# Optimization experiments

Measured on AMD Instinct MI355X. Metric: run time of the kernel, lower is better.

The kernel has to match this reference:

```python
import jax, jax.numpy as jnp
import numpy as np

EPS = 1e-12  # matches torch F.normalize default eps
K = 10       # knn size hardcoded in forward


def _l2_normalize(x, axis):
    n = jnp.linalg.norm(x, axis=axis, keepdims=True)
    return x / jnp.maximum(n, EPS)


def setup_inputs() -> dict:
    key = jax.random.key(0)
    k1, k2, k3, k4, k5 = jax.random.split(key, 5)
    BS, D, C = 4096, 768, 128
    NCLUST, CSIZE, NTRAIN, NCLS = 500, 100, 100000, 10
    train_embedding = jax.random.normal(k1, (BS, D), dtype=jnp.float32)
    # init_concept: uniform in [-0.5, 0.5]
    concept = jax.random.uniform(k2, (D, C), dtype=jnp.float32, minval=-0.5, maxval=0.5)
    clusters = jax.random.normal(k3, (NCLUST, CSIZE, D), dtype=jnp.float32)
    train_embeddings = jax.random.normal(k4, (NTRAIN, D), dtype=jnp.float32)
    w_hx = jax.random.normal(k5, (NCLS, D), dtype=jnp.float32) * 0.02
    b_hx = jnp.zeros((NCLS,), dtype=jnp.float32)
    return {"train_embedding": train_embedding, "concept": concept,
            "clusters": clusters, "train_embeddings": train_embeddings,
            "w_hx": w_hx, "b_hx": b_hx}


def reference(train_embedding, concept, clusters, train_embeddings, w_hx, b_hx):
    C = concept.shape[1]
    E = train_embeddings.T                       # (D, N) == self.train_embeddings

    concept_normalized = _l2_normalize(concept, axis=0)
    gram = concept.T @ concept                   # (C, C)
    proj_matrix = concept @ jnp.linalg.inv(gram) @ concept.T   # (D, D)
    proj = proj_matrix @ train_embedding.T       # (D, BS)

    cluster_mean = jnp.mean(clusters, axis=1)    # (NCLUST, D)
    score_matrix = jnp.abs(cluster_mean @ concept_normalized)  # (NCLUST, C)
    score_norm = _l2_normalize(score_matrix, axis=0)
    L_sparse_1_old = jnp.sum(score_norm)
    # sum_{i!=j} dot(score_norm[:,i], score_norm[:,j]) = sum(G) - trace(G)
    G = score_norm.T @ score_norm                # (C, C)
    L_sparse_2_old = jnp.sum(G) - jnp.trace(G)

    y_pred = proj.T @ w_hx.T + b_hx              # (BS, NCLS)

    # batched knn over all concepts: ||e - c||^2 = ||e||^2 - 2 c.e + ||c||^2
    e_sq = jnp.sum(E * E, axis=0)                # (N,)
    c_sq = jnp.sum(concept * concept, axis=0)    # (C,)
    d2 = e_sq[None, :] - 2.0 * (concept.T @ E) + c_sq[:, None]  # (C, N)
    _, knn_idx = jax.lax.top_k(-d2, K)           # (C, K) smallest distances
    knn_act = E[:, knn_idx]                      # (D, C, K)
    # per-concept sum(c * c_knn)/K, then mean over concepts
    L_sparse_1_new = jnp.mean(jnp.sum(concept[:, :, None] * knn_act, axis=(0, 2)) / K)

    all_concept_dot = concept.T @ concept        # (C, C)
    mask = 1.0 - jnp.eye(C, dtype=all_concept_dot.dtype)
    L_sparse_2_new = jnp.mean(all_concept_dot * mask)

    return (y_pred, L_sparse_1_old, L_sparse_2_old, L_sparse_1_new, L_sparse_2_new)
```

## Files before the change

kernel.cpp:

```cpp
#include <hip/hip_runtime.h>
#include <stdint.h>

#define M_TRAIN 100000
#define D_DIM   768
#define C_DIM   128
#define NCLUST  500
#define CSIZE   100
#define NCLS    10
#define KSEL    10
#define NCHUNK  4
#define CHUNKN  25000
#define CAND_PER 16
#define NCT     (NCHUNK * CAND_PER)
#define FLT_INF 3.402823466e38f

typedef __attribute__((ext_vector_type(8))) short bhalf8;
typedef __attribute__((ext_vector_type(4))) float f32x4;
typedef __attribute__((ext_vector_type(8))) unsigned short ushort8;
typedef __attribute__((ext_vector_type(4))) unsigned short ushort4v;

#define WS_KEYT   0LL
#define WS_BIMG   25600000LL
#define WS_CONT   25796608LL
#define WS_GRAM   26189824LL
#define WS_PSCORE 26255360LL
#define WS_CT     26767360LL
#define WS_CAND   26798080LL
#define WS_PSUM   26830848LL
#define WS_TSOL   26831360LL

#define GSTR 132

static __device__ __forceinline__ unsigned short f2bf(float f) {
    union { float f; unsigned int u; } x; x.f = f;
    unsigned int u = x.u;
    return (unsigned short)((u + 0x7fffu + ((u >> 16) & 1u)) >> 16);
}

__global__ void __launch_bounds__(256) kA(const float* __restrict__ cpt,
        const float* __restrict__ clus, float* __restrict__ conceptT,
        unsigned short* __restrict__ bimg, float* __restrict__ gram,
        float* __restrict__ pscore) {
    int b = blockIdx.x, t = threadIdx.x;
    if (b < 1000) {
        __shared__ float mean_s[D_DIM];
        int cl = b >> 1, h = b & 1;
        if (t < 192) {
            const float* base = clus + (long)cl * CSIZE * D_DIM + (long)h * 50 * D_DIM + t * 4;
            float ax = 0.f, ay = 0.f, az = 0.f, aw = 0.f;
            for (int s = 0; s < 50; s += 2) {
                float4 v0 = *(const float4*)(base + (long)s * D_DIM);
                float4 v1 = *(const float4*)(base + (long)(s + 1) * D_DIM);
                ax += v0.x + v1.x; ay += v0.y + v1.y;
                az += v0.z + v1.z; aw += v0.w + v1.w;
            }
            const float k = 1.0f / CSIZE;
            mean_s[t * 4 + 0] = ax * k; mean_s[t * 4 + 1] = ay * k;
            mean_s[t * 4 + 2] = az * k; mean_s[t * 4 + 3] = aw * k;
        }
        __syncthreads();
        if (t < 128) {
            float s = 0.f;
            #pragma unroll 4
            for (int d = 0; d < D_DIM; ++d) s += mean_s[d] * cpt[d * 128 + t];
            pscore[h * (NCLUST * 128) + cl * 128 + t] = s;
        }
    } else if (b < 1384) {
        int tid = (b - 1000) * 256 + t;
        int d = tid >> 7, c = tid & 127;
        float v = cpt[tid];
        conceptT[c * D_DIM + d] = v;
        int kc = d >> 6, kin = d & 63;
        int ofs = kc * 16384 + (((c << 7) + (kin << 1)) ^ ((c & 7) << 4));
        *(unsigned short*)((char*)bimg + ofs) = f2bf(v);
    } else {
        int c1 = (b - 1384) * 2 + (t >> 7);
        int c2 = t & 127;
        float s = 0.f;
        #pragma unroll 4
        for (int d = 0; d < D_DIM; ++d)
            s += cpt[d * 128 + c1] * cpt[d * 128 + c2];
        gram[c1 * 128 + c2] = s;
    }
}

__device__ __forceinline__ float blk_red256(float v, float* buf, int t) {
    #pragma unroll
    for (int m = 32; m > 0; m >>= 1) v += __shfl_xor(v, m);
    if ((t & 63) == 0) buf[t >> 6] = v;
    __syncthreads();
    return buf[0] + buf[1] + buf[2] + buf[3];
}

__device__ __forceinline__ void cg_role(char* smem, const float* __restrict__ gram,
        const float* __restrict__ cpt, const float* __restrict__ whx,
        float* __restrict__ tsol, float* __restrict__ out_l2new, int j) {
    float* G    = (float*)smem;
    float* p_s  = (float*)(smem + 67584);
    float* rbuf = (float*)(smem + 68096);
    int t = threadIdx.x;
    int r = t & 127;
    bool lo = (t < 128);
    if (lo) {
        #pragma unroll 8
        for (int c = 0; c < 128; c += 4)
            *(float4*)&G[r * GSTR + c] = *(const float4*)&gram[r * 128 + c];
    }
    const float* wj = whx + j * D_DIM;
    float rhs = 0.f;
    if (lo) {
        for (int d = 0; d < D_DIM; d += 4)
            rhs += cpt[(d + 0) * 128 + r] * wj[d + 0]
                 + cpt[(d + 1) * 128 + r] * wj[d + 1]
                 + cpt[(d + 2) * 128 + r] * wj[d + 2]
                 + cpt[(d + 3) * 128 + r] * wj[d + 3];
    }
    float x = 0.f, res = rhs, p = rhs;
    if (lo) p_s[r] = p;
    float rr = blk_red256(lo ? res * res : 0.f, rbuf, t);
    __syncthreads();
    if (j == 0) {
        float s = 0.f;
        if (lo) {
            #pragma unroll 8
            for (int c = 0; c < 128; ++c) s += G[r * GSTR + c];
            s -= G[r * GSTR + r];
        }
        float tot = blk_red256(s, rbuf + 8, t);
        if (t == 0) out_l2new[0] = tot / 16384.0f;
    }
    for (int it = 0; it < 20; ++it) {
        float q = 0.f;
        if (lo) {
            #pragma unroll 8
            for (int c = 0; c < 128; c += 4) {
                float4 g  = *(const float4*)&G[r * GSTR + c];
                float4 pp = *(const float4*)&p_s[c];
                q += g.x * pp.x + g.y * pp.y + g.z * pp.z + g.w * pp.w;
            }
        }
        float pq = blk_red256(lo ? p * q : 0.f, rbuf + 4, t);
        float alpha = rr / pq;
        x += alpha * p;
        res -= alpha * q;
        float rrn = blk_red256(lo ? res * res : 0.f, rbuf, t);
        float beta = rrn / rr;
        rr = rrn;
        p = res + beta * p;
        if (lo) p_s[r] = p;
        __syncthreads();
    }
    if (lo) tsol[r * NCLS + j] = x;
}

__device__ __forceinline__ void old_role(char* smem, const float* __restrict__ pscore,
        const float* __restrict__ gram, float* __restrict__ out01) {
    float* ss2     = (float*)smem;
    float* sm2     = (float*)(smem + 1024);
    float* rcn_s   = (float*)(smem + 2048);
    float* wcomb   = (float*)(smem + 2560);
    float* redA    = (float*)(smem + 3072);
    float* redB    = (float*)(smem + 3584);
    float* wred4   = (float*)(smem + 4096);
    float* trace_s = (float*)(smem + 4112);
    const float* p0 = pscore;
    const float* p1 = pscore + NCLUST * 128;
    int t = threadIdx.x;
    int c = t & 127, w2 = t >> 7;
    if (t < 128) rcn_s[t] = 1.0f / fmaxf(sqrtf(gram[t * 129]), 1e-12f);
    __syncthreads();
    float rc = rcn_s[c];
    float ss = 0.f, sm = 0.f;
    for (int bb = 0; bb < 25; ++bb) {
        float a[10];
        #pragma unroll
        for (int k = 0; k < 10; ++k) {
            int cl = w2 + 2 * (10 * bb + k);
            a[k] = p0[cl * 128 + c] + p1[cl * 128 + c];
        }
        #pragma unroll
        for (int k = 0; k < 10; ++k) { float v = fabsf(a[k]) * rc; ss += v * v; sm += v; }
    }
    ss2[w2 * 128 + c] = ss; sm2[w2 * 128 + c] = sm;
    __syncthreads();
    if (t < 128) {
        float S = ss2[t] + ss2[128 + t];
        float M = sm2[t] + sm2[128 + t];
        float nn = fmaxf(sqrtf(S), 1e-12f);
        float iv = 1.0f / nn;
        wcomb[t] = rcn_s[t] * iv;
        redA[t] = M * iv;
        redB[t] = S * iv * iv;
    }
    __syncthreads();
    if (t < 64) {
        float a = redA[t] + redA[t + 64];
        float b2 = redB[t] + redB[t + 64];
        #pragma unroll
        for (int m = 32; m > 0; m >>= 1) { a += __shfl_xor(a, m); b2 += __shfl_xor(b2, m); }
        if (t == 0) { out01[0] = a; trace_s[0] = b2; }
    }
    __syncthreads();
    int w = t >> 6, lane = t & 63;
    float wc0 = wcomb[lane], wc1 = wcomb[lane + 64];
    float rsq = 0.f;
    for (int bb = 0; bb < 25; ++bb) {
        float a0[5], a1[5];
        #pragma unroll
        for (int k = 0; k < 5; ++k) {
            int cl = w + 4 * (5 * bb + k);
            a0[k] = p0[cl * 128 + lane] + p1[cl * 128 + lane];
            a1[k] = p0[cl * 128 + 64 + lane] + p1[cl * 128 + 64 + lane];
        }
        #pragma unroll
        for (int k = 0; k < 5; ++k) {
            float v = fabsf(a0[k]) * wc0 + fabsf(a1[k]) * wc1;
            #pragma unroll
            for (int m = 32; m > 0; m >>= 1) v += __shfl_xor(v, m);
            if (lane == 0) rsq += v * v;
        }
    }
    if (lane == 0) wred4[w] = rsq;
    __syncthreads();
    if (t == 0) out01[1] = wred4[0] + wred4[1] + wred4[2] + wred4[3] - trace_s[0];
}

__device__ __forceinline__ void P_role(char* smem, const float* __restrict__ E,
        const unsigned short* __restrict__ bimg, unsigned short* __restrict__ keyT,
        int blk) {
    char* lds = smem;
    float* esq_s = (float*)(smem + 65536);
    unsigned short* cst = (unsigned short*)lds;

    int t = threadIdx.x;
    int rowbase = blk * 128;
    int lane = t & 63, w = t >> 6;
    int wr = w >> 1, wc = w & 1;
    f32x4 acc[4][4];
    #pragma unroll
    for (int m = 0; m < 4; ++m)
        #pragma unroll
        for (int n = 0; n < 4; ++n) acc[m][n] = (f32x4){0.f, 0.f, 0.f, 0.f};
    float esq_p[4] = {0.f, 0.f, 0.f, 0.f};
    int g = t >> 3, k8 = t & 7;

    float4 a0[4], a1[4];
    bhalf8 breg[4];

    auto stage_issue = [&](int ks) {
        #pragma unroll
        for (int p = 0; p < 4; ++p) {
            int grow = rowbase + 32 * p + g;
            if (grow < M_TRAIN) {
                const float* src = E + (long)grow * D_DIM + ks * 64 + k8 * 8;
                a0[p] = *(const float4*)(src);
                a1[p] = *(const float4*)(src + 4);
            } else {
                a0[p] = make_float4(0.f, 0.f, 0.f, 0.f);
                a1[p] = make_float4(0.f, 0.f, 0.f, 0.f);
            }
        }
        const char* bs = (const char*)bimg + ks * 16384;
        #pragma unroll
        for (int i = 0; i < 4; ++i)
            breg[i] = *(const bhalf8*)(bs + (i * 256 + t) * 16);
    };
    auto stage_write = [&](int buf) {
        char* Ab = lds + buf * 16384;
        char* Bb = lds + 32768 + buf * 16384;
        #pragma unroll
        for (int p = 0; p < 4; ++p) {
            int row = 32 * p + g;
            float4 v0 = a0[p], v1 = a1[p];
            esq_p[p] += v0.x*v0.x + v0.y*v0.y + v0.z*v0.z + v0.w*v0.w
                      + v1.x*v1.x + v1.y*v1.y + v1.z*v1.z + v1.w*v1.w;
            bhalf8 h;
            h[0] = (short)f2bf(v0.x); h[1] = (short)f2bf(v0.y);
            h[2] = (short)f2bf(v0.z); h[3] = (short)f2bf(v0.w);
            h[4] = (short)f2bf(v1.x); h[5] = (short)f2bf(v1.y);
            h[6] = (short)f2bf(v1.z); h[7] = (short)f2bf(v1.w);
            int byte = (row * 128 + k8 * 16) ^ ((row & 7) << 4);
            *(bhalf8*)(Ab + byte) = h;
        }
        #pragma unroll
        for (int i = 0; i < 4; ++i)
            *(bhalf8*)(Bb + (i * 256 + t) * 16) = breg[i];
    };

    stage_issue(0);
    stage_write(0);
    __syncthreads();
    int cur = 0;
    for (int ks = 0; ks < 12; ++ks) {
        if (ks < 11) stage_issue(ks + 1);
        const char* Ab = lds + cur * 16384;
        const char* Bb = lds + 32768 + cur * 16384;
        bhalf8 af[4][2], bf[4][2];
        int kb = (lane >> 4) * 16;
        #pragma unroll
        for (int m = 0; m < 4; ++m) {
            int row = wr * 64 + m * 16 + (lane & 15);
            int b0 = row * 128, sw = (row & 7) << 4;
            af[m][0] = *(const bhalf8*)(Ab + ((b0 + kb) ^ sw));
            af[m][1] = *(const bhalf8*)(Ab + ((b0 + kb + 64) ^ sw));
        }
        #pragma unroll
        for (int n = 0; n < 4; ++n) {
            int c = wc * 64 + n * 16 + (lane & 15);
            int b0 = c * 128, sw = (c & 7) << 4;
            bf[n][0] = *(const bhalf8*)(Bb + ((b0 + kb) ^ sw));
            bf[n][1] = *(const bhalf8*)(Bb + ((b0 + kb + 64) ^ sw));
        }
        #pragma unroll
        for (int m = 0; m < 4; ++m)
            #pragma unroll
            for (int n = 0; n < 4; ++n) {
                acc[m][n] = __builtin_amdgcn_mfma_f32_16x16x32_bf16(af[m][0], bf[n][0], acc[m][n], 0, 0, 0);
                acc[m][n] = __builtin_amdgcn_mfma_f32_16x16x32_bf16(af[m][1], bf[n][1], acc[m][n], 0, 0, 0);
            }
        if (ks < 11) stage_write(cur ^ 1);
        __syncthreads();
        cur ^= 1;
    }
    #pragma unroll
    for (int p = 0; p < 4; ++p) {
        float v = esq_p[p];
        v += __shfl_xor(v, 1); v += __shfl_xor(v, 2); v += __shfl_xor(v, 4);
        if (k8 == 0) esq_s[32 * p + g] = v;
    }
    __syncthreads();
    #pragma unroll
    for (int m = 0; m < 4; ++m) {
        int r0 = wr * 64 + m * 16 + (lane >> 4) * 4;
        float e0 = esq_s[r0], e1 = esq_s[r0 + 1], e2 = esq_s[r0 + 2], e3 = esq_s[r0 + 3];
        #pragma unroll
        for (int n = 0; n < 4; ++n) {
            int c = wc * 64 + n * 16 + (lane & 15);
            ushort4v kv;
            kv[0] = f2bf(e0 - 2.f * acc[m][n][0]);
            kv[1] = f2bf(e1 - 2.f * acc[m][n][1]);
            kv[2] = f2bf(e2 - 2.f * acc[m][n][2]);
            kv[3] = f2bf(e3 - 2.f * acc[m][n][3]);
            *(ushort4v*)(cst + c * 136 + r0) = kv;
        }
    }
    __syncthreads();
    #pragma unroll
    for (int it = 0; it < 8; ++it) {
        int c = w * 32 + it * 4 + (lane >> 4);
        int r = (lane & 15) * 8;
        if (rowbase + r < M_TRAIN) {
            ushort8 v = *(const ushort8*)(cst + c * 136 + r);
            *(ushort8*)(keyT + (long)c * M_TRAIN + rowbase + r) = v;
        }
    }
}

__global__ void __launch_bounds__(256, 2) kB(const float* __restrict__ E,
        const unsigned short* __restrict__ bimg, unsigned short* __restrict__ keyT,
        const float* __restrict__ gram, const float* __restrict__ cpt,
        const float* __restrict__ whx, float* __restrict__ tsol,
        float* __restrict__ out_scal, const float* __restrict__ pscore) {
    __shared__ __align__(16) char smem[68160];
    int b = blockIdx.x;
    if (b < 10)       cg_role(smem, gram, cpt, whx, tsol, out_scal + 3, b);
    else if (b == 10) old_role(smem, pscore, gram, out_scal);
    else              P_role(smem, E, bimg, keyT, b - 11);
}

__global__ void __launch_bounds__(256) kC(const unsigned short* __restrict__ keyT,
        int* __restrict__ cand, const float* __restrict__ cpt,
        const float* __restrict__ tsol, float* __restrict__ ct) {
    int b = blockIdx.x, t = threadIdx.x;
    if (b < 512) {
        __shared__ int sk[2048];
        __shared__ int si[2048];
        __shared__ int wk[4]; __shared__ int wi[4], wsl[4];
        int c = b >> 2, h = b & 3;
        const unsigned short* col = keyT + (long)c * M_TRAIN + h * CHUNKN;
        int base = h * CHUNKN;
        int tk[8], ti[8];
        #pragma unroll
        for (int i = 0; i < 8; ++i) { tk[i] = 0x7fffffff; ti[i] = 0x7fffffff; }
        for (int i = t; i < CHUNKN / 8; i += 256) {
            ushort8 v = *(const ushort8*)(col + i * 8);
            int idx = base + i * 8;
            #pragma unroll
            for (int q = 0; q < 8; ++q) {
                int cv = (int)v[q]; int ci = idx + q;
                if (cv < tk[7] || (cv == tk[7] && ci < ti[7])) {
                    #pragma unroll
                    for (int jj = 0; jj < 8; ++jj) {
                        bool sw = (cv < tk[jj]) || (cv == tk[jj] && ci < ti[jj]);
                        int ok = tk[jj]; int oi = ti[jj];
                        if (sw) { tk[jj] = cv; ti[jj] = ci; cv = ok; ci = oi; }
                    }
                }
            }
        }
        #pragma unroll
        for (int i = 0; i < 8; ++i) { sk[t * 8 + i] = tk[i]; si[t * 8 + i] = ti[i]; }
        __syncthreads();
        int lane = t & 63, w = t >> 6;
        for (int sel = 0; sel < CAND_PER; ++sel) {
            int bk = 0x7fffffff, bi = 0x7fffffff, bs = -1;
            #pragma unroll
            for (int i = 0; i < 8; ++i) {
                int s = t * 8 + i;
                int v = sk[s];
                if (v < bk || (v == bk && si[s] < bi)) { bk = v; bi = si[s]; bs = s; }
            }
            #pragma unroll
            for (int m = 32; m > 0; m >>= 1) {
                int ok = __shfl_xor(bk, m); int oi = __shfl_xor(bi, m); int os = __shfl_xor(bs, m);
                if (ok < bk || (ok == bk && oi < bi)) { bk = ok; bi = oi; bs = os; }
            }
            if (lane == 0) { wk[w] = bk; wi[w] = bi; wsl[w] = bs; }
            __syncthreads();
            if (t == 0) {
                int fk = wk[0], fi = wi[0], fs = wsl[0];
                for (int i = 1; i < 4; ++i)
                    if (wk[i] < fk || (wk[i] == fk && wi[i] < fi)) { fk = wk[i]; fi = wi[i]; fs = wsl[i]; }
                cand[(c * NCHUNK + h) * CAND_PER + sel] = fi;
                sk[fs] = 0x7fffffff; si[fs] = 0x7fffffff;
            }
            __syncthreads();
        }
    } else {
        int idx = (b - 512) * 256 + t;
        int d = idx / NCLS, j = idx - d * NCLS;
        const float* crow = cpt + d * 128;
        float s = 0.f;
        #pragma unroll 4
        for (int c = 0; c < 128; ++c) s += crow[c] * tsol[c * NCLS + j];
        ct[idx] = s;
    }
}

__global__ void __launch_bounds__(256) kD(const float* __restrict__ te,
        const float* __restrict__ ct, const float* __restrict__ bhx,
        float* __restrict__ out, const float* __restrict__ E,
        const float* __restrict__ conceptT, const int* __restrict__ cand,
        float* __restrict__ psum) {
    int b = blockIdx.x, t = threadIdx.x;
    if (b < 512) {
        __shared__ float ctT[NCLS][D_DIM];
        for (int o = t; o < D_DIM * NCLS; o += 256) {
            int j = o / D_DIM, d = o % D_DIM;
            ctT[j][d] = ct[d * NCLS + j];
        }
        __syncthreads();
        int r = t >> 5, l = t & 31;
        long row = (long)b * 8 + r;
        const float* er = te + row * D_DIM;
        float acc[NCLS];
        #pragma unroll
        for (int j = 0; j < NCLS; ++j) acc[j] = 0.f;
        for (int d0 = l * 4; d0 < D_DIM; d0 += 128) {
            float4 e = *(const float4*)(er + d0);
            #pragma unroll
            for (int j = 0; j < NCLS; ++j) {
                float4 cc = *(const float4*)(&ctT[j][d0]);
                acc[j] += e.x*cc.x + e.y*cc.y + e.z*cc.z + e.w*cc.w;
            }
        }
        #pragma unroll
        for (int j = 0; j < NCLS; ++j) {
            #pragma unroll
            for (int m = 16; m > 0; m >>= 1) acc[j] += __shfl_xor(acc[j], m);
        }
        if (l == 0) {
            #pragma unroll
            for (int j = 0; j < NCLS; ++j) out[row * NCLS + j] = acc[j] + bhx[j];
        }
    } else {
        __shared__ float skey[NCT], sdot[NCT];
        __shared__ int sidx[NCT];
        int c = b - 512;
        int g = t >> 2, l4 = t & 3;
        int idx = cand[c * NCT + g];
        const float* er = E + (long)idx * D_DIM;
        const float* cr = conceptT + c * D_DIM;
        float dot = 0.f, ss = 0.f;
        for (int d0 = l4 * 4; d0 < D_DIM; d0 += 16) {
            float4 e = *(const float4*)(er + d0);
            float4 cc = *(const float4*)(cr + d0);
            dot += e.x*cc.x + e.y*cc.y + e.z*cc.z + e.w*cc.w;
            ss  += e.x*e.x + e.y*e.y + e.z*e.z + e.w*e.w;
        }
        dot += __shfl_xor(dot, 1); dot += __shfl_xor(dot, 2);
        ss  += __shfl_xor(ss, 1);  ss  += __shfl_xor(ss, 2);
        if (l4 == 0) { skey[g] = ss - 2.f * dot; sdot[g] = dot; sidx[g] = idx; }
        __syncthreads();
        if (t == 0) {
            float sum = 0.f;
            unsigned long long used = 0ull;
            for (int s = 0; s < KSEL; ++s) {
                float bk = FLT_INF; int bi = 0x7fffffff, bs = 0;
                for (int i = 0; i < NCT; ++i) {
                    if ((used >> i) & 1ull) continue;
                    if (skey[i] < bk || (skey[i] == bk && sidx[i] < bi)) { bk = skey[i]; bi = sidx[i]; bs = i; }
                }
                used |= (1ull << bs);
                sum += sdot[bs];
            }
            psum[c] = sum;
        }
    }
}

__global__ void k_finalize(const float* __restrict__ psum, float* __restrict__ out2) {
    __shared__ float red[128];
    int t = threadIdx.x;
    red[t] = psum[t];
    __syncthreads();
    for (int s = 64; s > 0; s >>= 1) { if (t < s) red[t] += red[t + s]; __syncthreads(); }
    if (t == 0) out2[0] = red[0] * (1.0f / (C_DIM * KSEL));
}

extern "C" void kernel_launch(void* const* d_in, const int* in_sizes, int n_in,
                              void* d_out, int out_size, void* d_ws, size_t ws_size,
                              hipStream_t stream) {
    (void)in_sizes; (void)n_in; (void)out_size; (void)ws_size;
    const float* te   = (const float*)d_in[0];
    const float* cpt  = (const float*)d_in[1];
    const float* clus = (const float*)d_in[2];
    const float* tes  = (const float*)d_in[3];
    const float* whx  = (const float*)d_in[4];
    const float* bhx  = (const float*)d_in[5];
    float* out = (float*)d_out;
    char* ws = (char*)d_ws;
    unsigned short* keyT  = (unsigned short*)(ws + WS_KEYT);
    unsigned short* bimg  = (unsigned short*)(ws + WS_BIMG);
    float* conceptT       = (float*)(ws + WS_CONT);
    float* gram           = (float*)(ws + WS_GRAM);
    float* pscore         = (float*)(ws + WS_PSCORE);
    float* ct             = (float*)(ws + WS_CT);
    int* cand             = (int*)(ws + WS_CAND);
    float* psum           = (float*)(ws + WS_PSUM);
    float* tsol           = (float*)(ws + WS_TSOL);

    kA<<<dim3(1448), dim3(256), 0, stream>>>(cpt, clus, conceptT, bimg, gram, pscore);
    kB<<<dim3(793),  dim3(256), 0, stream>>>(tes, bimg, keyT, gram, cpt, whx, tsol,
                                             out + 40960, pscore);
    kC<<<dim3(542),  dim3(256), 0, stream>>>(keyT, cand, cpt, tsol, ct);
    kD<<<dim3(640),  dim3(256), 0, stream>>>(te, ct, bhx, out, tes, conceptT, cand, psum);
    k_finalize<<<dim3(1), dim3(128), 0, stream>>>(psum, out + 40962);
}
```

Before: 336.7 us.

## Move ct computation into CG blocks, fuse y_pred into kC, packed bf16 conversion

Each CG block now computes its column of ct = concept·x right after solving, so kC no longer needs extra blocks for it. The y_pred GEMV blocks move from kD into kC, where they run alongside the candidate-selection blocks, and kD keeps only the knn rescoring. The scalar float-to-bf16 rounding is replaced with the packed bf16x2 intrinsic. This cuts the cross-kernel dependency chain and lets independent work overlap, at the cost of extra serial work in the 10 CG blocks.

Measured after the change: 335.4 us. No clear change (-0.4%).

```diff
diff --git a/kernel.cpp b/kernel.cpp
--- a/kernel.cpp
+++ b/kernel.cpp
@@ -1,4 +1,5 @@
 #include <hip/hip_runtime.h>
+#include <hip/hip_bf16.h>
 #include <stdint.h>
 
 #define M_TRAIN 100000
@@ -35,6 +36,11 @@
     union { float f; unsigned int u; } x; x.f = f;
     unsigned int u = x.u;
     return (unsigned short)((u + 0x7fffu + ((u >> 16) & 1u)) >> 16);
+}
+static __device__ __forceinline__ unsigned int f2bf2(float lo, float hi) {
+    union { __hip_bfloat162 h; unsigned int u; } cv;
+    cv.h = __float22bfloat162_rn(make_float2(lo, hi));
+    return cv.u;
 }
 
 __global__ void __launch_bounds__(256) kA(const float* __restrict__ cpt,
@@ -94,7 +100,8 @@
 
 __device__ __forceinline__ void cg_role(char* smem, const float* __restrict__ gram,
         const float* __restrict__ cpt, const float* __restrict__ whx,
-        float* __restrict__ tsol, float* __restrict__ out_l2new, int j) {
+        float* __restrict__ tsol, float* __restrict__ ct,
+        float* __restrict__ out_l2new, int j) {
     float* G    = (float*)smem;
     float* p_s  = (float*)(smem + 67584);
     float* rbuf = (float*)(smem + 68096);
@@ -151,6 +158,19 @@
         __syncthreads();
     }
     if (lo) tsol[r * NCLS + j] = x;
+    if (lo) p_s[r] = x;
+    __syncthreads();
+    for (int d = t; d < D_DIM; d += 256) {
+        const float* crow = cpt + d * 128;
+        float s = 0.f;
+        #pragma unroll 8
+        for (int c = 0; c < 128; c += 4) {
+            float4 cc = *(const float4*)(crow + c);
+            float4 xx = *(const float4*)&p_s[c];
+            s += cc.x * xx.x + cc.y * xx.y + cc.z * xx.z + cc.w * xx.w;
+        }
+        ct[d * NCLS + j] = s;
+    }
 }
 
 __device__ __forceinline__ void old_role(char* smem, const float* __restrict__ pscore,
@@ -274,13 +294,13 @@
             float4 v0 = a0[p], v1 = a1[p];
             esq_p[p] += v0.x*v0.x + v0.y*v0.y + v0.z*v0.z + v0.w*v0.w
                       + v1.x*v1.x + v1.y*v1.y + v1.z*v1.z + v1.w*v1.w;
-            bhalf8 h;
-            h[0] = (short)f2bf(v0.x); h[1] = (short)f2bf(v0.y);
-            h[2] = (short)f2bf(v0.z); h[3] = (short)f2bf(v0.w);
-            h[4] = (short)f2bf(v1.x); h[5] = (short)f2bf(v1.y);
-            h[6] = (short)f2bf(v1.z); h[7] = (short)f2bf(v1.w);
+            union { bhalf8 v; unsigned int u[4]; } h;
+            h.u[0] = f2bf2(v0.x, v0.y);
+            h.u[1] = f2bf2(v0.z, v0.w);
+            h.u[2] = f2bf2(v1.x, v1.y);
+            h.u[3] = f2bf2(v1.z, v1.w);
             int byte = (row * 128 + k8 * 16) ^ ((row & 7) << 4);
-            *(bhalf8*)(Ab + byte) = h;
+            *(bhalf8*)(Ab + byte) = h.v;
         }
         #pragma unroll
         for (int i = 0; i < 4; ++i)
@@ -336,12 +356,10 @@
         #pragma unroll
         for (int n = 0; n < 4; ++n) {
             int c = wc * 64 + n * 16 + (lane & 15);
-            ushort4v kv;
-            kv[0] = f2bf(e0 - 2.f * acc[m][n][0]);
-            kv[1] = f2bf(e1 - 2.f * acc[m][n][1]);
-            kv[2] = f2bf(e2 - 2.f * acc[m][n][2]);
-            kv[3] = f2bf(e3 - 2.f * acc[m][n][3]);
-            *(ushort4v*)(cst + c * 136 + r0) = kv;
+            union { ushort4v v; unsigned int u[2]; } kv;
+            kv.u[0] = f2bf2(e0 - 2.f * acc[m][n][0], e1 - 2.f * acc[m][n][1]);
+            kv.u[1] = f2bf2(e2 - 2.f * acc[m][n][2], e3 - 2.f * acc[m][n][3]);
+            *(ushort4v*)(cst + c * 136 + r0) = kv.v;
         }
     }
     __syncthreads();
@@ -360,22 +378,27 @@
         const unsigned short* __restrict__ bimg, unsigned short* __restrict__ keyT,
         const float* __restrict__ gram, const float* __restrict__ cpt,
         const float* __restrict__ whx, float* __restrict__ tsol,
-        float* __restrict__ out_scal, const float* __restrict__ pscore) {
+        float* __restrict__ ct, float* __restrict__ out_scal,
+        const float* __restrict__ pscore) {
     __shared__ __align__(16) char smem[68160];
     int b = blockIdx.x;
-    if (b < 10)       cg_role(smem, gram, cpt, whx, tsol, out_scal + 3, b);
+    if (b < 10)       cg_role(smem, gram, cpt, whx, tsol, ct, out_scal + 3, b);
     else if (b == 10) old_role(smem, pscore, gram, out_scal);
     else              P_role(smem, E, bimg, keyT, b - 11);
 }
 
 __global__ void __launch_bounds__(256) kC(const unsigned short* __restrict__ keyT,
-        int* __restrict__ cand, const float* __restrict__ cpt,
-        const float* __restrict__ tsol, float* __restrict__ ct) {
+        int* __restrict__ cand, const float* __restrict__ te,
+        const float* __restrict__ ct, const float* __restrict__ bhx,
+        float* __restrict__ out) {
+    __shared__ __align__(16) char smem[30720];
     int b = blockIdx.x, t = threadIdx.x;
     if (b < 512) {
-        __shared__ int sk[2048];
-        __shared__ int si[2048];
-        __shared__ int wk[4]; __shared__ int wi[4], wsl[4];
+        int* sk  = (int*)smem;
+        int* si  = (int*)(smem + 8192);
+        int* wk  = (int*)(smem + 16384);
+        int* wi  = (int*)(smem + 16400);
+        int* wsl = (int*)(smem + 16416);
         int c = b >> 2, h = b & 3;
         const unsigned short* col = keyT + (long)c * M_TRAIN + h * CHUNKN;
         int base = h * CHUNKN;
@@ -427,31 +450,14 @@
             __syncthreads();
         }
     } else {
-        int idx = (b - 512) * 256 + t;
-        int d = idx / NCLS, j = idx - d * NCLS;
-        const float* crow = cpt + d * 128;
-        float s = 0.f;
-        #pragma unroll 4
-        for (int c = 0; c < 128; ++c) s += crow[c] * tsol[c * NCLS + j];
-        ct[idx] = s;
-    }
-}
-
-__global__ void __launch_bounds__(256) kD(const float* __restrict__ te,
-        const float* __restrict__ ct, const float* __restrict__ bhx,
-        float* __restrict__ out, const float* __restrict__ E,
-        const float* __restrict__ conceptT, const int* __restrict__ cand,
-        float* __restrict__ psum) {
-    int b = blockIdx.x, t = threadIdx.x;
-    if (b < 512) {
-        __shared__ float ctT[NCLS][D_DIM];
+        float* ctT = (float*)smem;
         for (int o = t; o < D_DIM * NCLS; o += 256) {
             int j = o / D_DIM, d = o % D_DIM;
-            ctT[j][d] = ct[d * NCLS + j];
+            ctT[j * D_DIM + d] = ct[d * NCLS + j];
         }
         __syncthreads();
         int r = t >> 5, l = t & 31;
-        long row = (long)b * 8 + r;
+        long row = (long)(b - 512) * 8 + r;
         const float* er = te + row * D_DIM;
         float acc[NCLS];
         #pragma unroll
@@ -460,7 +466,7 @@
             float4 e = *(const float4*)(er + d0);
             #pragma unroll
             for (int j = 0; j < NCLS; ++j) {
-                float4 cc = *(const float4*)(&ctT[j][d0]);
+                float4 cc = *(const float4*)(&ctT[j * D_DIM + d0]);
                 acc[j] += e.x*cc.x + e.y*cc.y + e.z*cc.z + e.w*cc.w;
             }
         }
@@ -473,39 +479,43 @@
             #pragma unroll
             for (int j = 0; j < NCLS; ++j) out[row * NCLS + j] = acc[j] + bhx[j];
         }
-    } else {
-        __shared__ float skey[NCT], sdot[NCT];
-        __shared__ int sidx[NCT];
-        int c = b - 512;
-        int g = t >> 2, l4 = t & 3;
-        int idx = cand[c * NCT + g];
-        const float* er = E + (long)idx * D_DIM;
-        const float* cr = conceptT + c * D_DIM;
-        float dot = 0.f, ss = 0.f;
-        for (int d0 = l4 * 4; d0 < D_DIM; d0 += 16) {
-            float4 e = *(const float4*)(er + d0);
-            float4 cc = *(const float4*)(cr + d0);
-            dot += e.x*cc.x + e.y*cc.y + e.z*cc.z + e.w*cc.w;
-            ss  += e.x*e.x + e.y*e.y + e.z*e.z + e.w*e.w;
-        }
-        dot += __shfl_xor(dot, 1); dot += __shfl_xor(dot, 2);
-        ss  += __shfl_xor(ss, 1);  ss  += __shfl_xor(ss, 2);
-        if (l4 == 0) { skey[g] = ss - 2.f * dot; sdot[g] = dot; sidx[g] = idx; }
-        __syncthreads();
-        if (t == 0) {
-            float sum = 0.f;
-            unsigned long long used = 0ull;
-            for (int s = 0; s < KSEL; ++s) {
-                float bk = FLT_INF; int bi = 0x7fffffff, bs = 0;
-                for (int i = 0; i < NCT; ++i) {
-                    if ((used >> i) & 1ull) continue;
-                    if (skey[i] < bk || (skey[i] == bk && sidx[i] < bi)) { bk = skey[i]; bi = sidx[i]; bs = i; }
-                }
-                used |= (1ull << bs);
-                sum += sdot[bs];
-            }
-            psum[c] = sum;
-        }
+    }
+}
+
+__global__ void __launch_bounds__(256) kD(const float* __restrict__ E,
+        const float* __restrict__ conceptT, const int* __restrict__ cand,
+        float* __restrict__ psum) {
+    __shared__ float skey[NCT], sdot[NCT];
+    __shared__ int sidx[NCT];
+    int c = blockIdx.x, t = threadIdx.x;
+    int g = t >> 2, l4 = t & 3;
+    int idx = cand[c * NCT + g];
+    const float* er = E + (long)idx * D_DIM;
+    const float* cr = conceptT + c * D_DIM;
+    float dot = 0.f, ss = 0.f;
+    for (int d0 = l4 * 4; d0 < D_DIM; d0 += 16) {
+        float4 e = *(const float4*)(er + d0);
+        float4 cc = *(const float4*)(cr + d0);
+        dot += e.x*cc.x + e.y*cc.y + e.z*cc.z + e.w*cc.w;
+        ss  += e.x*e.x + e.y*e.y + e.z*e.z + e.w*e.w;
+    }
+    dot += __shfl_xor(dot, 1); dot += __shfl_xor(dot, 2);
+    ss  += __shfl_xor(ss, 1);  ss  += __shfl_xor(ss, 2);
+    if (l4 == 0) { skey[g] = ss - 2.f * dot; sdot[g] = dot; sidx[g] = idx; }
+    __syncthreads();
+    if (t == 0) {
+        float sum = 0.f;
+        unsigned long long used = 0ull;
+        for (int s = 0; s < KSEL; ++s) {
+            float bk = FLT_INF; int bi = 0x7fffffff, bs = 0;
+            for (int i = 0; i < NCT; ++i) {
+                if ((used >> i) & 1ull) continue;
+                if (skey[i] < bk || (skey[i] == bk && sidx[i] < bi)) { bk = skey[i]; bi = sidx[i]; bs = i; }
+            }
+            used |= (1ull << bs);
+            sum += sdot[bs];
+        }
+        psum[c] = sum;
     }
 }
 
@@ -541,9 +551,9 @@
     float* tsol           = (float*)(ws + WS_TSOL);
 
     kA<<<dim3(1448), dim3(256), 0, stream>>>(cpt, clus, conceptT, bimg, gram, pscore);
-    kB<<<dim3(793),  dim3(256), 0, stream>>>(tes, bimg, keyT, gram, cpt, whx, tsol,
+    kB<<<dim3(793),  dim3(256), 0, stream>>>(tes, bimg, keyT, gram, cpt, whx, tsol, ct,
                                              out + 40960, pscore);
-    kC<<<dim3(542),  dim3(256), 0, stream>>>(keyT, cand, cpt, tsol, ct);
-    kD<<<dim3(640),  dim3(256), 0, stream>>>(te, ct, bhx, out, tes, conceptT, cand, psum);
+    kC<<<dim3(1024), dim3(256), 0, stream>>>(keyT, cand, te, ct, bhx, out);
+    kD<<<dim3(128),  dim3(256), 0, stream>>>(tes, conceptT, cand, psum);
     k_finalize<<<dim3(1), dim3(128), 0, stream>>>(psum, out + 40962);
 }
```
